# Performance work log

Hardware: AMD Instinct MI355X
Metric: run time of the kernel (lower is better)

The kernel has to match this reference:

```python
import jax, jax.numpy as jnp
import numpy as np

WIRES = 4

def _ry(theta):
    # theta: scalar or (N,) -> (2,2) or (N,2,2) complex64
    c = jnp.cos(theta / 2)
    s = jnp.sin(theta / 2)
    return jnp.stack([jnp.stack([c, -s], -1), jnp.stack([s, c], -1)], -2).astype(jnp.complex64)

def _rz(phi):
    e = jnp.exp(-0.5j * phi.astype(jnp.complex64))
    z = jnp.zeros_like(e)
    return jnp.stack([jnp.stack([e, z], -1), jnp.stack([z, jnp.conj(e)], -1)], -2)

def _apply(state, U, w):
    # state: (N,2,2,2,2); wire w lives on axis 1+w
    state = jnp.moveaxis(state, 1 + w, -1)
    if U.ndim == 2:
        state = jnp.einsum('ij,n...j->n...i', U, state)
    else:
        state = jnp.einsum('nij,n...j->n...i', U, state)
    return jnp.moveaxis(state, -1, 1 + w)

def _cnot(state, c, t):
    # flip target axis where control axis == 1
    s0, s1 = jnp.split(state, 2, axis=1 + c)
    s1 = jnp.flip(s1, axis=1 + t)
    return jnp.concatenate([s0, s1], axis=1 + c)

def _quanv(patches, q_params):
    # patches: (N,4) angles; q_params: (L,4,3). Batched 4-qubit statevector sim.
    N = patches.shape[0]
    state = jnp.zeros((N, 16), jnp.complex64).at[:, 0].set(1.0).reshape(N, 2, 2, 2, 2)
    num_layers = q_params.shape[0]
    for i in range(num_layers):
        for w in range(WIRES):
            state = _apply(state, _ry(patches[:, w]), w)
        for w in range(WIRES):
            state = _cnot(state, w, (w + 1) % WIRES)
        for w in range(WIRES):
            state = _apply(state, _rz(q_params[i, w, 0]), w)
            state = _apply(state, _ry(q_params[i, w, 1]), w)
            state = _apply(state, _rz(q_params[i, w, 2]), w)
    probs = jnp.abs(state) ** 2  # (N,2,2,2,2)
    zsign = jnp.array([1.0, -1.0], jnp.float32)
    ez = [jnp.sum(probs * zsign.reshape((1,) + (1,) * w + (2,) + (1,) * (WIRES - 1 - w)),
                  axis=(1, 2, 3, 4)) for w in range(WIRES)]
    return jnp.stack(ez, -1)  # (N,4) <Z_j> expectations

def setup_inputs() -> dict:
    key = jax.random.key(0)
    k1, k2, k3 = jax.random.split(key, 3)
    B = 1024
    x = jax.random.normal(k1, (B, 1, 28, 28), dtype=jnp.float32)
    q_params = jax.random.normal(k2, (3, 4, 3), dtype=jnp.float32)
    W = jax.random.normal(k3, (10, 784), dtype=jnp.float32) * 0.03
    b = jnp.zeros((10,), jnp.float32)
    return {"x": x, "q_params": q_params, "W": W, "b": b}

def reference(x, q_params, W, b):
    B = x.shape[0]
    # extract 2x2 patches in (row-block, col-block) order, each flattened row-major
    patches = x.reshape(B, 14, 2, 14, 2).transpose(0, 1, 3, 2, 4).reshape(B * 196, 4)
    feats = _quanv(patches, q_params).reshape(B, 196 * 4)  # cat order: patch-major, 4 wires each
    logits = feats @ W.T + b
    return jax.nn.log_softmax(logits, axis=-1)
```

## Files before the change

### kernel.cpp

```cpp
#include <hip/hip_runtime.h>
#include <math.h>


#define APPLY_RY(ST, cc, ss) do { \
  _Pragma("unroll") \
  for (int i = 0; i < 16; ++i) { \
    if (!(i & (ST))) { \
      float ar = sr[i], ai = si[i], br = sr[i + (ST)], bi = si[i + (ST)]; \
      sr[i]        = (cc) * ar - (ss) * br; \
      si[i]        = (cc) * ai - (ss) * bi; \
      sr[i + (ST)] = (ss) * ar + (cc) * br; \
      si[i + (ST)] = (ss) * ai + (cc) * bi; \
    } } } while (0)

#define APPLY_CNOT(SC, ST) do { \
  _Pragma("unroll") \
  for (int i = 0; i < 16; ++i) { \
    if ((i & (SC)) && !(i & (ST))) { \
      float tr = sr[i], ti = si[i]; \
      sr[i] = sr[i + (ST)]; si[i] = si[i + (ST)]; \
      sr[i + (ST)] = tr;    si[i + (ST)] = ti; \
    } } } while (0)

#define APPLY_U(ST, U0R, U0I, U1R, U1I) do { \
  _Pragma("unroll") \
  for (int i = 0; i < 16; ++i) { \
    if (!(i & (ST))) { \
      float ar = sr[i], ai = si[i], br = sr[i + (ST)], bi = si[i + (ST)]; \
      sr[i]        =  (U0R) * ar - (U0I) * ai + (U1R) * br - (U1I) * bi; \
      si[i]        =  (U0R) * ai + (U0I) * ar + (U1R) * bi + (U1I) * br; \
      sr[i + (ST)] = -(U1R) * ar - (U1I) * ai + (U0R) * br + (U0I) * bi; \
      si[i + (ST)] = -(U1R) * ai + (U1I) * ar + (U0R) * bi - (U0I) * br; \
    } } } while (0)

#define APPLY_U_LDS(ST, l, w) do { \
  const float* u_ = &uu[((l) * 4 + (w)) * 4]; \
  float u0r = u_[0], u0i = u_[1], u1r = u_[2], u1i = u_[3]; \
  APPLY_U(ST, u0r, u0i, u1r, u1i); \
} while (0)

#define LAYER_TAIL(l) do { \
  APPLY_CNOT(8, 4); APPLY_CNOT(4, 2); APPLY_CNOT(2, 1); APPLY_CNOT(1, 8); \
  APPLY_U_LDS(8, l, 0); APPLY_U_LDS(4, l, 1); APPLY_U_LDS(2, l, 2); APPLY_U_LDS(1, l, 3); \
} while (0)

#define DATA_RY_ALL() do { \
  APPLY_RY(8, dc[0], ds[0]); APPLY_RY(4, dc[1], ds[1]); \
  APPLY_RY(2, dc[2], ds[2]); APPLY_RY(1, dc[3], ds[3]); \
} while (0)

template <int LC>
__global__ __launch_bounds__(256, 4) void quanv_fused_kernel(
    const float* __restrict__ x,
    const float* __restrict__ qp,
    const float* __restrict__ W,
    const float* __restrict__ bias,
    float* __restrict__ out,
    int Lrt)
{
  const int L = (LC > 0) ? LC : Lrt;
  const int n   = blockIdx.x;
  const int tid = threadIdx.x;
  const int p   = tid;

  __shared__ float uu[8 * 16];
  if (tid < 4 * L) {
    const int l = tid >> 2, w = tid & 3;
    const float p0 = qp[l * 12 + w * 3 + 0];
    const float p1 = qp[l * 12 + w * 3 + 1];
    const float p2 = qp[l * 12 + w * 3 + 2];
    float c, s, ca, sa, cb, sb;
    __sincosf(0.5f * p1, &s, &c);
    __sincosf(0.5f * (p0 + p2), &sa, &ca);
    __sincosf(0.5f * (p0 - p2), &sb, &cb);
    float* u_ = &uu[(l * 4 + w) * 4];
    u_[0] =  c * ca;
    u_[1] = -c * sa;
    u_[2] = -s * cb;
    u_[3] = -s * sb;
  }
  __syncthreads();

  float ez[4] = {0.f, 0.f, 0.f, 0.f};

  if (p < 196) {
    const int pr = p / 14, pcc = p % 14;
    const float2* xb = (const float2*)(x + (size_t)n * 784 + (2 * pr) * 28 + 2 * pcc);
    float2 top = xb[0], bot = xb[14];
    float dc[4], ds[4];
    __sincosf(0.5f * top.x, &ds[0], &dc[0]);
    __sincosf(0.5f * top.y, &ds[1], &dc[1]);
    __sincosf(0.5f * bot.x, &ds[2], &dc[2]);
    __sincosf(0.5f * bot.y, &ds[3], &dc[3]);

    float sr[16], si[16];

    if (LC > 0) {
      float p00 = dc[0] * dc[1], p01 = dc[0] * ds[1];
      float p10 = ds[0] * dc[1], p11 = ds[0] * ds[1];
      float q00 = dc[2] * dc[3], q01 = dc[2] * ds[3];
      float q10 = ds[2] * dc[3], q11 = ds[2] * ds[3];
      float hi[4] = {p00, p01, p10, p11};
      float lo[4] = {q00, q01, q10, q11};
#pragma unroll
      for (int i = 0; i < 16; ++i) { sr[i] = hi[i >> 2] * lo[i & 3]; si[i] = 0.f; }
      LAYER_TAIL(0);
#pragma unroll
      for (int l = 1; l < ((LC > 0) ? LC : 1); ++l) {
        DATA_RY_ALL();
        LAYER_TAIL(l);
      }
    } else {
#pragma unroll
      for (int i = 0; i < 16; ++i) { sr[i] = 0.f; si[i] = 0.f; }
      sr[0] = 1.f;
      for (int l = 0; l < L; ++l) {
        DATA_RY_ALL();
        LAYER_TAIL(l);
      }
    }

#pragma unroll
    for (int i = 0; i < 16; ++i) {
      float pp = sr[i] * sr[i] + si[i] * si[i];
      ez[0] += (i & 8) ? -pp : pp;
      ez[1] += (i & 4) ? -pp : pp;
      ez[2] += (i & 2) ? -pp : pp;
      ez[3] += (i & 1) ? -pp : pp;
    }
  }

  float part[10];
#pragma unroll
  for (int c = 0; c < 10; ++c) part[c] = 0.f;
  if (p < 196) {
    const float4* Wv = (const float4*)W;
#pragma unroll
    for (int c = 0; c < 10; ++c) {
      float4 wc = Wv[c * 196 + p];
      part[c] = ez[0] * wc.x + ez[1] * wc.y + ez[2] * wc.z + ez[3] * wc.w;
    }
  }

  const int lane = tid & 63;
  const int wave = tid >> 6;
  __shared__ float red[4][10];
#pragma unroll
  for (int c = 0; c < 10; ++c) {
    float v = part[c];
#pragma unroll
    for (int off = 32; off > 0; off >>= 1) v += __shfl_down(v, off, 64);
    if (lane == 0) red[wave][c] = v;
  }
  __syncthreads();

  if (tid == 0) {
    float logits[10];
    float m = -1e30f;
#pragma unroll
    for (int c = 0; c < 10; ++c) {
      logits[c] = red[0][c] + red[1][c] + red[2][c] + red[3][c] + bias[c];
      m = fmaxf(m, logits[c]);
    }
    float sum = 0.f;
#pragma unroll
    for (int c = 0; c < 10; ++c) sum += __expf(logits[c] - m);
    float lse = m + __logf(sum);
#pragma unroll
    for (int c = 0; c < 10; ++c) out[(size_t)n * 10 + c] = logits[c] - lse;
  }
}

extern "C" void kernel_launch(void* const* d_in, const int* in_sizes, int n_in,
                              void* d_out, int out_size, void* d_ws, size_t ws_size,
                              hipStream_t stream) {
  const float* x    = (const float*)d_in[0];
  const float* qp   = (const float*)d_in[1];
  const float* W    = (const float*)d_in[2];
  const float* bias = (const float*)d_in[3];
  float* out        = (float*)d_out;

  const int B = in_sizes[0] / 784;
  const int L = in_sizes[1] / 12;

  switch (L) {
    case 1: quanv_fused_kernel<1><<<B, 256, 0, stream>>>(x, qp, W, bias, out, L); break;
    case 2: quanv_fused_kernel<2><<<B, 256, 0, stream>>>(x, qp, W, bias, out, L); break;
    case 3: quanv_fused_kernel<3><<<B, 256, 0, stream>>>(x, qp, W, bias, out, L); break;
    case 4: quanv_fused_kernel<4><<<B, 256, 0, stream>>>(x, qp, W, bias, out, L); break;
    default: quanv_fused_kernel<0><<<B, 256, 0, stream>>>(x, qp, W, bias, out, L); break;
  }
}
```

Before: 81.33 us.

## Fuse data RY into per-layer SU2 and fold last layer into Z observables

Reorders the circuit so the first layer's data RY and CNOT ring act on a real product state. Each later layer's data RY is merged with the previous layer's parameterized SU2 into one 2x2 gate. The final layer's unitary is absorbed analytically into rotated Z observables computed once per block, which removes a full layer of gate applications per patch. Parameter setup moves to idle threads 196 and up. In exchange the expectation step becomes costlier, and the algebraic rewrite is harder to verify.

```diff
diff --git a/kernel.cpp b/kernel.cpp
--- a/kernel.cpp
+++ b/kernel.cpp
@@ -2,27 +2,7 @@
 #include <math.h>
 
 
-#define APPLY_RY(ST, cc, ss) do { \
-  _Pragma("unroll") \
-  for (int i = 0; i < 16; ++i) { \
-    if (!(i & (ST))) { \
-      float ar = sr[i], ai = si[i], br = sr[i + (ST)], bi = si[i + (ST)]; \
-      sr[i]        = (cc) * ar - (ss) * br; \
-      si[i]        = (cc) * ai - (ss) * bi; \
-      sr[i + (ST)] = (ss) * ar + (cc) * br; \
-      si[i + (ST)] = (ss) * ai + (cc) * bi; \
-    } } } while (0)
-
-#define APPLY_CNOT(SC, ST) do { \
-  _Pragma("unroll") \
-  for (int i = 0; i < 16; ++i) { \
-    if ((i & (SC)) && !(i & (ST))) { \
-      float tr = sr[i], ti = si[i]; \
-      sr[i] = sr[i + (ST)]; si[i] = si[i + (ST)]; \
-      sr[i + (ST)] = tr;    si[i + (ST)] = ti; \
-    } } } while (0)
-
-#define APPLY_U(ST, U0R, U0I, U1R, U1I) do { \
+#define APPLY_SU2(ST, U0R, U0I, U1R, U1I) do { \
   _Pragma("unroll") \
   for (int i = 0; i < 16; ++i) { \
     if (!(i & (ST))) { \
@@ -33,20 +13,52 @@
       si[i + (ST)] = -(U1R) * ai + (U1I) * ar + (U0R) * bi - (U0I) * br; \
     } } } while (0)
 
-#define APPLY_U_LDS(ST, l, w) do { \
+#define APPLY_CNOT_C(SC, ST) do { \
+  _Pragma("unroll") \
+  for (int i = 0; i < 16; ++i) { \
+    if ((i & (SC)) && !(i & (ST))) { \
+      float tr = sr[i], ti = si[i]; \
+      sr[i] = sr[i + (ST)]; si[i] = si[i + (ST)]; \
+      sr[i + (ST)] = tr;    si[i + (ST)] = ti; \
+    } } } while (0)
+
+#define APPLY_CNOT_R(SC, ST) do { \
+  _Pragma("unroll") \
+  for (int i = 0; i < 16; ++i) { \
+    if ((i & (SC)) && !(i & (ST))) { \
+      float tr = rr[i]; rr[i] = rr[i + (ST)]; rr[i + (ST)] = tr; \
+    } } } while (0)
+
+#define CNOT_RING_C() do { \
+  APPLY_CNOT_C(8, 4); APPLY_CNOT_C(4, 2); APPLY_CNOT_C(2, 1); APPLY_CNOT_C(1, 8); \
+} while (0)
+
+#define FUSE_V(l, w) do { \
   const float* u_ = &uu[((l) * 4 + (w)) * 4]; \
-  float u0r = u_[0], u0i = u_[1], u1r = u_[2], u1i = u_[3]; \
-  APPLY_U(ST, u0r, u0i, u1r, u1i); \
+  float fu0r = u_[0], fu0i = u_[1], fu1r = u_[2], fu1i = u_[3]; \
+  float cw = dc[w], sw = ds[w]; \
+  v0r = cw * fu0r + sw * fu1r; \
+  v0i = cw * fu0i - sw * fu1i; \
+  v1r = cw * fu1r - sw * fu0r; \
+  v1i = cw * fu1i + sw * fu0i; \
 } while (0)
 
-#define LAYER_TAIL(l) do { \
-  APPLY_CNOT(8, 4); APPLY_CNOT(4, 2); APPLY_CNOT(2, 1); APPLY_CNOT(1, 8); \
-  APPLY_U_LDS(8, l, 0); APPLY_U_LDS(4, l, 1); APPLY_U_LDS(2, l, 2); APPLY_U_LDS(1, l, 3); \
-} while (0)
-
-#define DATA_RY_ALL() do { \
-  APPLY_RY(8, dc[0], ds[0]); APPLY_RY(4, dc[1], ds[1]); \
-  APPLY_RY(2, dc[2], ds[2]); APPLY_RY(1, dc[3], ds[3]); \
+#define APPLY_SU2_REAL0() do { \
+  _Pragma("unroll") \
+  for (int i = 0; i < 8; ++i) { \
+    float a_ = rr[i], b_ = rr[i + 8]; \
+    sr[i]     = v0r * a_ + v1r * b_; \
+    si[i]     = v0i * a_ + v1i * b_; \
+    sr[i + 8] = v0r * b_ - v1r * a_; \
+    si[i + 8] = v1i * a_ - v0i * b_; \
+  } } while (0)
+
+#define LAYER_V_FULL(l) do { \
+  FUSE_V(l, 0); APPLY_SU2(8, v0r, v0i, v1r, v1i); \
+  FUSE_V(l, 1); APPLY_SU2(4, v0r, v0i, v1r, v1i); \
+  FUSE_V(l, 2); APPLY_SU2(2, v0r, v0i, v1r, v1i); \
+  FUSE_V(l, 3); APPLY_SU2(1, v0r, v0i, v1r, v1i); \
+  CNOT_RING_C(); \
 } while (0)
 
 template <int LC>
@@ -64,8 +76,11 @@
   const int p   = tid;
 
   __shared__ float uu[8 * 16];
-  if (tid < 4 * L) {
-    const int l = tid >> 2, w = tid & 3;
+  __shared__ float mm[16];
+
+  if (tid >= 196 && tid < 196 + 4 * L) {
+    const int k = tid - 196;
+    const int l = k >> 2, w = k & 3;
     const float p0 = qp[l * 12 + w * 3 + 0];
     const float p1 = qp[l * 12 + w * 3 + 1];
     const float p2 = qp[l * 12 + w * 3 + 2];
@@ -73,11 +88,17 @@
     __sincosf(0.5f * p1, &s, &c);
     __sincosf(0.5f * (p0 + p2), &sa, &ca);
     __sincosf(0.5f * (p0 - p2), &sb, &cb);
-    float* u_ = &uu[(l * 4 + w) * 4];
-    u_[0] =  c * ca;
-    u_[1] = -c * sa;
-    u_[2] = -s * cb;
-    u_[3] = -s * sb;
+    const float u0r =  c * ca, u0i = -c * sa;
+    const float u1r = -s * cb, u1i = -s * sb;
+    if (l < L - 1) {
+      float* u_ = &uu[(l * 4 + w) * 4];
+      u_[0] = u0r; u_[1] = u0i; u_[2] = u1r; u_[3] = u1i;
+    } else {
+      float* m_ = &mm[w * 4];
+      m_[0] = u0r * u0r + u0i * u0i - u1r * u1r - u1i * u1i;
+      m_[1] = 4.f * (u0r * u1r + u0i * u1i);
+      m_[2] = 4.f * (u0r * u1i - u0i * u1r);
+    }
   }
   __syncthreads();
 
@@ -93,40 +114,53 @@
     __sincosf(0.5f * bot.x, &ds[2], &dc[2]);
     __sincosf(0.5f * bot.y, &ds[3], &dc[3]);
 
+    float rr[16];
+    {
+      float hi[4] = {dc[0]*dc[1], dc[0]*ds[1], ds[0]*dc[1], ds[0]*ds[1]};
+      float lo[4] = {dc[2]*dc[3], dc[2]*ds[3], ds[2]*dc[3], ds[2]*ds[3]};
+#pragma unroll
+      for (int i = 0; i < 16; ++i) rr[i] = hi[i >> 2] * lo[i & 3];
+    }
+    APPLY_CNOT_R(8, 4); APPLY_CNOT_R(4, 2); APPLY_CNOT_R(2, 1); APPLY_CNOT_R(1, 8);
+
     float sr[16], si[16];
-
-    if (LC > 0) {
-      float p00 = dc[0] * dc[1], p01 = dc[0] * ds[1];
-      float p10 = ds[0] * dc[1], p11 = ds[0] * ds[1];
-      float q00 = dc[2] * dc[3], q01 = dc[2] * ds[3];
-      float q10 = ds[2] * dc[3], q11 = ds[2] * ds[3];
-      float hi[4] = {p00, p01, p10, p11};
-      float lo[4] = {q00, q01, q10, q11};
-#pragma unroll
-      for (int i = 0; i < 16; ++i) { sr[i] = hi[i >> 2] * lo[i & 3]; si[i] = 0.f; }
-      LAYER_TAIL(0);
-#pragma unroll
-      for (int l = 1; l < ((LC > 0) ? LC : 1); ++l) {
-        DATA_RY_ALL();
-        LAYER_TAIL(l);
+    float v0r, v0i, v1r, v1i;
+
+    if (L >= 2) {
+      FUSE_V(0, 0); APPLY_SU2_REAL0();
+      FUSE_V(0, 1); APPLY_SU2(4, v0r, v0i, v1r, v1i);
+      FUSE_V(0, 2); APPLY_SU2(2, v0r, v0i, v1r, v1i);
+      FUSE_V(0, 3); APPLY_SU2(1, v0r, v0i, v1r, v1i);
+      CNOT_RING_C();
+      if (LC > 0) {
+#pragma unroll
+        for (int l = 1; l < LC - 1; ++l) LAYER_V_FULL(l);
+      } else {
+        for (int l = 1; l < L - 1; ++l) LAYER_V_FULL(l);
       }
     } else {
 #pragma unroll
-      for (int i = 0; i < 16; ++i) { sr[i] = 0.f; si[i] = 0.f; }
-      sr[0] = 1.f;
-      for (int l = 0; l < L; ++l) {
-        DATA_RY_ALL();
-        LAYER_TAIL(l);
+      for (int i = 0; i < 16; ++i) { sr[i] = rr[i]; si[i] = 0.f; }
+    }
+
+    float pp_[16];
+#pragma unroll
+    for (int i = 0; i < 16; ++i) pp_[i] = sr[i] * sr[i] + si[i] * si[i];
+#pragma unroll
+    for (int w = 0; w < 4; ++w) {
+      const int ST = 8 >> w;
+      const float aw = mm[w * 4 + 0], Br = mm[w * 4 + 1], Bi = mm[w * 4 + 2];
+      float e = 0.f;
+#pragma unroll
+      for (int i = 0; i < 16; ++i) {
+        if (!(i & ST)) {
+          const int j = i + ST;
+          float xr = sr[i] * sr[j] + si[i] * si[j];
+          float xi = sr[i] * si[j] - si[i] * sr[j];
+          e += aw * (pp_[i] - pp_[j]) + Br * xr - Bi * xi;
+        }
       }
-    }
-
-#pragma unroll
-    for (int i = 0; i < 16; ++i) {
-      float pp = sr[i] * sr[i] + si[i] * si[i];
-      ez[0] += (i & 8) ? -pp : pp;
-      ez[1] += (i & 4) ? -pp : pp;
-      ez[2] += (i & 2) ? -pp : pp;
-      ez[3] += (i & 1) ? -pp : pp;
+      ez[w] = e;
     }
   }
 
```

Measured after the change: 83.07 us. 2.1% more time.
